# Kernel tuning notes

Measured on AMD Instinct MI355X. Metric: run time of the kernel, lower is better.

## Reference

```python
import jax, jax.numpy as jnp
import numpy as np

B, S, D, H = 2, 2048, 1024, 16
HD = D // H
NEG = -9e15


def setup_inputs() -> dict:
    key = jax.random.key(0)
    ks = jax.random.split(key, 4)
    x = jax.random.normal(ks[0], (B, S, D), dtype=jnp.float32)
    # causal mask, broadcastable over batch and heads
    mask = jnp.tril(jnp.ones((S, S), dtype=jnp.int32))[None, None]
    W_qkv = jax.random.normal(ks[1], (D, 3 * D), dtype=jnp.float32) * (1.0 / np.sqrt(D))
    b_qkv = jnp.zeros((3 * D,), dtype=jnp.float32)
    W_out = jax.random.normal(ks[2], (D, D), dtype=jnp.float32) * (1.0 / np.sqrt(D))
    b_out = jnp.zeros((D,), dtype=jnp.float32)
    return {"x": x, "mask": mask, "W_qkv": W_qkv, "b_qkv": b_qkv,
            "W_out": W_out, "b_out": b_out}


def reference(x, mask, W_qkv, b_qkv, W_out, b_out):
    b, s, _ = x.shape
    qkv = x @ W_qkv + b_qkv                       # [B,S,3D]
    qkv = qkv.reshape(b, s, H, 3 * HD)            # per-head interleaved qkv
    qkv = jnp.transpose(qkv, (0, 2, 1, 3))        # [B,H,S,3*HD]
    q, k, v = jnp.split(qkv, 3, axis=-1)          # each [B,H,S,HD]
    scores = jnp.einsum('bhqd,bhkd->bhqk', q, k) / np.sqrt(HD)
    scores = jnp.where(mask == 0, jnp.float32(NEG), scores)
    attn = jax.nn.softmax(scores, axis=-1)
    out = jnp.einsum('bhqk,bhkd->bhqd', attn, v)  # [B,H,S,HD]
    out = jnp.transpose(out, (0, 2, 1, 3)).reshape(b, s, H * HD)
    return out @ W_out + b_out
```

## Files before the change

kernel.cpp:

```cpp
#include <hip/hip_runtime.h>
#include <math.h>

constexpr int Bb = 2, Ss = 2048, Dd = 1024, Hh = 16, HDd = 64;

typedef __attribute__((ext_vector_type(8))) short bf16x8;
typedef __attribute__((ext_vector_type(4))) float f32x4;
typedef __attribute__((ext_vector_type(8))) unsigned short u16x8;
typedef __attribute__((ext_vector_type(4))) unsigned short u16x4;

__device__ __forceinline__ unsigned short bf16_rn(float f) {
  unsigned int u = __float_as_uint(f);
  u += 0x7fffu + ((u >> 16) & 1u);
  return (unsigned short)(u >> 16);
}
__device__ __forceinline__ float bf16_f(unsigned short h) {
  return __uint_as_float(((unsigned int)h) << 16);
}

__global__ __launch_bounds__(256) void split_f32(
    const float* __restrict__ in, unsigned short* __restrict__ hi,
    unsigned short* __restrict__ lo, int n8) {
  int i = blockIdx.x * 256 + threadIdx.x;
  if (i >= n8) return;
  const float4* p = (const float4*)in + (size_t)i * 2;
  float4 a = p[0], b = p[1];
  float v[8] = {a.x, a.y, a.z, a.w, b.x, b.y, b.z, b.w};
  u16x8 h, l;
  #pragma unroll
  for (int j = 0; j < 8; j++) {
    unsigned short hb = bf16_rn(v[j]);
    h[j] = hb;
    l[j] = bf16_rn(v[j] - bf16_f(hb));
  }
  *(u16x8*)(hi + (size_t)i * 8) = h;
  *(u16x8*)(lo + (size_t)i * 8) = l;
}

__global__ __launch_bounds__(256) void transpose_split_f32(
    const float* __restrict__ W, unsigned short* __restrict__ Thi,
    unsigned short* __restrict__ Tlo, int K, int N) {
  __shared__ float tile[32][33];
  int n0 = blockIdx.x * 32, k0 = blockIdx.y * 32;
  int t = threadIdx.x;
  #pragma unroll
  for (int p = 0; p < 4; p++) {
    int idx = t + p * 256;
    int kk = idx >> 5, nn = idx & 31;
    tile[kk][nn] = W[(size_t)(k0 + kk) * N + n0 + nn];
  }
  __syncthreads();
  #pragma unroll
  for (int p = 0; p < 4; p++) {
    int idx = t + p * 256;
    int nn = idx >> 5, kk = idx & 31;
    float v = tile[kk][nn];
    unsigned short hb = bf16_rn(v);
    size_t o = (size_t)(n0 + nn) * K + k0 + kk;
    Thi[o] = hb;
    Tlo[o] = bf16_rn(v - bf16_f(hb));
  }
}

typedef __attribute__((address_space(3))) unsigned int lds_u32;
typedef const __attribute__((address_space(1))) unsigned int glb_u32;
__device__ __forceinline__ void gload16(const void* g, void* l) {
  __builtin_amdgcn_global_load_lds((glb_u32*)g, (lds_u32*)l, 16, 0, 0);
}

__device__ __forceinline__ void syncb() {
  asm volatile("" ::: "memory");
  __builtin_amdgcn_s_barrier();
  asm volatile("" ::: "memory");
}
template<int N> __device__ __forceinline__ void wait_vmcnt() {
  if constexpr (N == 0)      asm volatile("s_waitcnt vmcnt(0)" ::: "memory");
  else if constexpr (N == 4) asm volatile("s_waitcnt vmcnt(4)" ::: "memory");
  else if constexpr (N == 7) asm volatile("s_waitcnt vmcnt(7)" ::: "memory");
}

template<int BM, int BN>
__device__ __forceinline__ void gemm_core256(
    const unsigned short* __restrict__ Ahi, const unsigned short* __restrict__ Alo,
    const unsigned short* __restrict__ Bhi, const unsigned short* __restrict__ Blo,
    int KD, f32x4 (&acc)[BM / 32][BN / 64])
{
  constexpr int MF = BM / 32, NF = BN / 64;
  constexpr int NA = BM / 64, NB = BN / 64;
  constexpr int NV = NA + NB;
  constexpr int AELT = 2 * BM * 32;
  constexpr int BELT = 2 * BN * 32;
  constexpr int ALO = BM * 32, BLO = BN * 32;
  __shared__ unsigned short lds[2][AELT + BELT];

  const int tid = threadIdx.x, lane = tid & 63, wid = tid >> 6;
  const int m0 = blockIdx.y * BM, n0 = blockIdx.x * BN;
  const int wrow = wid >> 2, wcol = wid & 3;
  const int lrow = lane & 15, g = lane >> 4;

  const unsigned short* srcA[NA]; int dstA[NA];
  #pragma unroll
  for (int i = 0; i < NA; i++) {
    int gi = tid + i * 512;
    int lr = gi >> 2, s = gi & 3, gs = s ^ ((lr >> 1) & 3);
    const unsigned short* bp = (lr < BM) ? Ahi : Alo;
    int row = (lr < BM) ? lr : lr - BM;
    srcA[i] = bp + (size_t)(m0 + row) * KD + gs * 8;
    dstA[i] = (gi & ~63) * 8;
  }
  const unsigned short* srcB[NB]; int dstB[NB];
  #pragma unroll
  for (int i = 0; i < NB; i++) {
    int gi = tid + i * 512;
    int lr = gi >> 2, s = gi & 3, gs = s ^ ((lr >> 1) & 3);
    const unsigned short* bp = (lr < BN) ? Bhi : Blo;
    int row = (lr < BN) ? lr : lr - BN;
    srcB[i] = bp + (size_t)(n0 + row) * KD + gs * 8;
    dstB[i] = AELT + (gi & ~63) * 8;
  }

  int offA[MF], offB[NF];
  #pragma unroll
  for (int m = 0; m < MF; m++) {
    int row = wrow * (BM / 2) + m * 16 + lrow;
    offA[m] = row * 32 + ((g ^ ((row >> 1) & 3)) * 8);
  }
  #pragma unroll
  for (int n = 0; n < NF; n++) {
    int row = wcol * (BN / 4) + n * 16 + lrow;
    offB[n] = AELT + row * 32 + ((g ^ ((row >> 1) & 3)) * 8);
  }

  #pragma unroll
  for (int m = 0; m < MF; m++)
    #pragma unroll
    for (int n = 0; n < NF; n++) acc[m][n] = (f32x4){0.f, 0.f, 0.f, 0.f};

  const int nk = KD / 32;

  #pragma unroll
  for (int i = 0; i < NA; i++) gload16(srcA[i], &lds[0][dstA[i]]);
  #pragma unroll
  for (int i = 0; i < NB; i++) gload16(srcB[i], &lds[0][dstB[i]]);
  #pragma unroll
  for (int i = 0; i < NA; i++) gload16(srcA[i] + 32, &lds[1][dstA[i]]);
  #pragma unroll
  for (int i = 0; i < NB; i++) gload16(srcB[i] + 32, &lds[1][dstB[i]]);
  wait_vmcnt<NV>();
  syncb();

  for (int t = 0; t < nk; ++t) {
    const unsigned short* L = lds[t & 1];

    bf16x8 bh[NF], bl[NF];
    #pragma unroll
    for (int n = 0; n < NF; n++) {
      bh[n] = *(const bf16x8*)(L + offB[n]);
      bl[n] = *(const bf16x8*)(L + offB[n] + BLO);
    }
    {
      bf16x8 ah[MF / 2], al[MF / 2];
      #pragma unroll
      for (int m = 0; m < MF / 2; m++) {
        ah[m] = *(const bf16x8*)(L + offA[m]);
        al[m] = *(const bf16x8*)(L + offA[m] + ALO);
      }
      __builtin_amdgcn_s_setprio(1);
      #pragma unroll
      for (int m = 0; m < MF / 2; m++)
        #pragma unroll
        for (int n = 0; n < NF; n++) {
          acc[m][n] = __builtin_amdgcn_mfma_f32_16x16x32_bf16(ah[m], bh[n], acc[m][n], 0, 0, 0);
          acc[m][n] = __builtin_amdgcn_mfma_f32_16x16x32_bf16(ah[m], bl[n], acc[m][n], 0, 0, 0);
          acc[m][n] = __builtin_amdgcn_mfma_f32_16x16x32_bf16(al[m], bh[n], acc[m][n], 0, 0, 0);
        }
      __builtin_amdgcn_s_setprio(0);
    }
    syncb();
    {
      bf16x8 ah[MF / 2], al[MF / 2];
      #pragma unroll
      for (int m = 0; m < MF / 2; m++) {
        ah[m] = *(const bf16x8*)(L + offA[m + MF / 2]);
        al[m] = *(const bf16x8*)(L + offA[m + MF / 2] + ALO);
      }
      __builtin_amdgcn_s_setprio(1);
      #pragma unroll
      for (int m = 0; m < MF / 2; m++)
        #pragma unroll
        for (int n = 0; n < NF; n++) {
          acc[m + MF / 2][n] = __builtin_amdgcn_mfma_f32_16x16x32_bf16(ah[m], bh[n], acc[m + MF / 2][n], 0, 0, 0);
          acc[m + MF / 2][n] = __builtin_amdgcn_mfma_f32_16x16x32_bf16(ah[m], bl[n], acc[m + MF / 2][n], 0, 0, 0);
          acc[m + MF / 2][n] = __builtin_amdgcn_mfma_f32_16x16x32_bf16(al[m], bh[n], acc[m + MF / 2][n], 0, 0, 0);
        }
      __builtin_amdgcn_s_setprio(0);
    }

    if (t + 1 < nk) {
      asm volatile("s_waitcnt lgkmcnt(0)" ::: "memory");
      syncb();
      if (t + 2 < nk) {
        const int koff = (t + 2) * 32;
        unsigned short* W = lds[t & 1];
        #pragma unroll
        for (int i = 0; i < NA; i++) gload16(srcA[i] + koff, W + dstA[i]);
        #pragma unroll
        for (int i = 0; i < NB; i++) gload16(srcB[i] + koff, W + dstB[i]);
        wait_vmcnt<NV>();
      } else {
        wait_vmcnt<0>();
      }
      syncb();
    }
  }
}

__global__ __launch_bounds__(512) void gemm_qkv256(
    const unsigned short* __restrict__ Ahi, const unsigned short* __restrict__ Alo,
    const unsigned short* __restrict__ Bhi, const unsigned short* __restrict__ Blo,
    const float* __restrict__ bias,
    unsigned short* __restrict__ Qh, unsigned short* __restrict__ Ql,
    unsigned short* __restrict__ Kh, unsigned short* __restrict__ Kl,
    unsigned short* __restrict__ Vth, unsigned short* __restrict__ Vtl)
{
  f32x4 acc[8][3];
  gemm_core256<256, 192>(Ahi, Alo, Bhi, Blo, 1024, acc);

  const int tid = threadIdx.x, lane = tid & 63, wid = tid >> 6;
  const int lrow = lane & 15, g = lane >> 4;
  const int m0 = blockIdx.y * 256, n0 = blockIdx.x * 192;
  const int wrow = wid >> 2, wcol = wid & 3;
  const int bidx = m0 >> 11;
  const int sbase = (m0 & 2047) + wrow * 128 + g * 4;
  #pragma unroll
  for (int n = 0; n < 3; n++) {
    int gcol = n0 + wcol * 48 + n * 16 + lrow;
    unsigned hh = (unsigned)gcol / 192u;
    int inner = gcol - (int)hh * 192;
    int part = inner >> 6;
    int d = inner & 63;
    float bv = bias[gcol];
    size_t base = (size_t)(bidx * 16 + (int)hh) * 131072;
    #pragma unroll
    for (int m = 0; m < 8; m++) {
      f32x4 a = acc[m][n];
      int s0 = sbase + m * 16;
      if (part == 0) {
        #pragma unroll
        for (int r = 0; r < 4; r++) {
          float v = (a[r] + bv) * 0.18033688011112042f;
          unsigned short hi = bf16_rn(v);
          size_t ix = base + (size_t)(s0 + r) * 64 + d;
          Qh[ix] = hi; Ql[ix] = bf16_rn(v - bf16_f(hi));
        }
      } else if (part == 1) {
        #pragma unroll
        for (int r = 0; r < 4; r++) {
          float v = a[r] + bv;
          unsigned short hi = bf16_rn(v);
          size_t ix = base + (size_t)(s0 + r) * 64 + d;
          Kh[ix] = hi; Kl[ix] = bf16_rn(v - bf16_f(hi));
        }
      } else {
        u16x4 hv, lv;
        #pragma unroll
        for (int r = 0; r < 4; r++) {
          float v = a[r] + bv;
          hv[r] = bf16_rn(v);
          lv[r] = bf16_rn(v - bf16_f(hv[r]));
        }
        size_t ix = base + (size_t)d * 2048 + s0;
        *(u16x4*)(Vth + ix) = hv;
        *(u16x4*)(Vtl + ix) = lv;
      }
    }
  }
}

__global__ __launch_bounds__(512) void gemm_out256(
    const unsigned short* __restrict__ Ahi, const unsigned short* __restrict__ Alo,
    const unsigned short* __restrict__ Bhi, const unsigned short* __restrict__ Blo,
    const float* __restrict__ bias, float* __restrict__ C)
{
  f32x4 acc[4][2];
  gemm_core256<128, 128>(Ahi, Alo, Bhi, Blo, 1024, acc);

  const int tid = threadIdx.x, lane = tid & 63, wid = tid >> 6;
  const int lrow = lane & 15, g = lane >> 4;
  const int m0 = blockIdx.y * 128, n0 = blockIdx.x * 128;
  const int wrow = wid >> 2, wcol = wid & 3;
  #pragma unroll
  for (int n = 0; n < 2; n++) {
    int gcol = n0 + wcol * 32 + n * 16 + lrow;
    float bv = bias[gcol];
    #pragma unroll
    for (int m = 0; m < 4; m++) {
      f32x4 a = acc[m][n];
      #pragma unroll
      for (int r = 0; r < 4; r++) {
        int grow = m0 + wrow * 64 + m * 16 + g * 4 + r;
        C[(size_t)grow * 1024 + gcol] = a[r] + bv;
      }
    }
  }
}

__global__ __launch_bounds__(512) void flash_attn_mfma(
    const unsigned short* __restrict__ Qh, const unsigned short* __restrict__ Ql,
    const unsigned short* __restrict__ Kh, const unsigned short* __restrict__ Kl,
    const unsigned short* __restrict__ Vth, const unsigned short* __restrict__ Vtl,
    unsigned short* __restrict__ atthi, unsigned short* __restrict__ attlo)
{
  const int pidx = blockIdx.x;
  const int h = blockIdx.y, b = blockIdx.z;
  const int bh = b * Hh + h;
  const int NT = Ss / 128;
  const int qtA = pidx, qtB = NT - 1 - pidx;
  const int tid = threadIdx.x, lane = tid & 63, wid = tid >> 6;
  const int q0w = (wid < 4) ? (qtA * 128 + wid * 32)
                            : (qtB * 128 + (wid - 4) * 32);
  const int lrow = lane & 15, lg = lane >> 4;

  __shared__ unsigned short KH[2][4096], KL[2][4096], VH[2][4096], VL[2][4096];
  __shared__ unsigned short Pbuf[8][2048];

  const size_t hb = (size_t)bh * 131072;
  const unsigned short* qhb = Qh + hb;
  const unsigned short* qlb = Ql + hb;
  const unsigned short* khb = Kh + hb;
  const unsigned short* klb = Kl + hb;
  const unsigned short* vhb = Vth + hb;
  const unsigned short* vlb = Vtl + hb;

  bf16x8 qfh[2][2], qfl[2][2];
  #pragma unroll
  for (int mi = 0; mi < 2; mi++)
    #pragma unroll
    for (int ks = 0; ks < 2; ks++) {
      int off = (q0w + mi * 16 + lrow) * 64 + ks * 32 + lg * 8;
      qfh[mi][ks] = *(const bf16x8*)(qhb + off);
      qfl[mi][ks] = *(const bf16x8*)(qlb + off);
    }

  int offK[4][2], offP[2][2];
  #pragma unroll
  for (int ci = 0; ci < 4; ci++)
    #pragma unroll
    for (int ks = 0; ks < 2; ks++) {
      int row = ci * 16 + lrow;
      offK[ci][ks] = row * 64 + (((ks * 4 + lg) ^ (row & 7)) * 8);
    }
  #pragma unroll
  for (int mi = 0; mi < 2; mi++)
    #pragma unroll
    for (int ks = 0; ks < 2; ks++) {
      int row = mi * 16 + lrow;
      offP[mi][ks] = row * 64 + (((ks * 4 + lg) ^ (row & 7)) * 8);
    }

  const int sr = tid >> 3, sg = ((tid & 7) ^ ((tid >> 3) & 7)) * 8;

  float m_[2][4], l_[2][4];
  f32x4 oacc[2][4];
  #pragma unroll
  for (int mi = 0; mi < 2; mi++)
    #pragma unroll
    for (int r = 0; r < 4; r++) { m_[mi][r] = -INFINITY; l_[mi][r] = 0.f; }
  #pragma unroll
  for (int mi = 0; mi < 2; mi++)
    #pragma unroll
    for (int di = 0; di < 4; di++) oacc[mi][di] = (f32x4){0.f, 0.f, 0.f, 0.f};

  unsigned short* Pw = Pbuf[wid];
  const int nt = 2 * (qtB + 1);

  gload16(khb + (size_t)sr * 64 + sg, KH[0] + wid * 512);
  gload16(klb + (size_t)sr * 64 + sg, KL[0] + wid * 512);
  gload16(vhb + (size_t)sr * 2048 + sg, VH[0] + wid * 512);
  gload16(vlb + (size_t)sr * 2048 + sg, VL[0] + wid * 512);
  __syncthreads();

  for (int t = 0; t < nt; ++t) {
    const int kv0 = t * 64;
    if (t + 1 < nt) {
      const int nb = (t + 1) & 1;
      const int nk = kv0 + 64;
      gload16(khb + (size_t)(nk + sr) * 64 + sg, KH[nb] + wid * 512);
      gload16(klb + (size_t)(nk + sr) * 64 + sg, KL[nb] + wid * 512);
      gload16(vhb + (size_t)sr * 2048 + nk + sg, VH[nb] + wid * 512);
      gload16(vlb + (size_t)sr * 2048 + nk + sg, VL[nb] + wid * 512);
    }

    if (kv0 <= q0w + 31) {
      const int cb = t & 1;
      const unsigned short* KHc = KH[cb];
      const unsigned short* KLc = KL[cb];
      const unsigned short* VHc = VH[cb];
      const unsigned short* VLc = VL[cb];

      f32x4 sf[2][4];
      #pragma unroll
      for (int mi = 0; mi < 2; mi++)
        #pragma unroll
        for (int ci = 0; ci < 4; ci++) sf[mi][ci] = (f32x4){0.f, 0.f, 0.f, 0.f};
      __builtin_amdgcn_s_setprio(1);
      #pragma unroll
      for (int ci = 0; ci < 4; ci++) {
        bf16x8 kh0 = *(const bf16x8*)(KHc + offK[ci][0]);
        bf16x8 kh1 = *(const bf16x8*)(KHc + offK[ci][1]);
        bf16x8 kl0 = *(const bf16x8*)(KLc + offK[ci][0]);
        bf16x8 kl1 = *(const bf16x8*)(KLc + offK[ci][1]);
        #pragma unroll
        for (int mi = 0; mi < 2; mi++) {
          f32x4 s = sf[mi][ci];
          s = __builtin_amdgcn_mfma_f32_16x16x32_bf16(qfh[mi][0], kh0, s, 0, 0, 0);
          s = __builtin_amdgcn_mfma_f32_16x16x32_bf16(qfh[mi][1], kh1, s, 0, 0, 0);
          s = __builtin_amdgcn_mfma_f32_16x16x32_bf16(qfh[mi][0], kl0, s, 0, 0, 0);
          s = __builtin_amdgcn_mfma_f32_16x16x32_bf16(qfh[mi][1], kl1, s, 0, 0, 0);
          s = __builtin_amdgcn_mfma_f32_16x16x32_bf16(qfl[mi][0], kh0, s, 0, 0, 0);
          s = __builtin_amdgcn_mfma_f32_16x16x32_bf16(qfl[mi][1], kh1, s, 0, 0, 0);
          sf[mi][ci] = s;
        }
      }
      __builtin_amdgcn_s_setprio(0);

      if (kv0 + 63 > q0w) {
        #pragma unroll
        for (int mi = 0; mi < 2; mi++)
          #pragma unroll
          for (int ci = 0; ci < 4; ci++)
            #pragma unroll
            for (int r = 0; r < 4; r++) {
              int q = q0w + mi * 16 + lg * 4 + r;
              int kv = kv0 + ci * 16 + lrow;
              if (kv > q) sf[mi][ci][r] = -1e30f;
            }
      }

      #pragma unroll
      for (int mi = 0; mi < 2; mi++)
        #pragma unroll
        for (int r = 0; r < 4; r++) {
          float mx = fmaxf(fmaxf(sf[mi][0][r], sf[mi][1][r]),
                           fmaxf(sf[mi][2][r], sf[mi][3][r]));
          mx = fmaxf(mx, __shfl_xor(mx, 1));
          mx = fmaxf(mx, __shfl_xor(mx, 2));
          mx = fmaxf(mx, __shfl_xor(mx, 4));
          mx = fmaxf(mx, __shfl_xor(mx, 8));
          float mn = fmaxf(m_[mi][r], mx);
          float alpha = __builtin_amdgcn_exp2f(m_[mi][r] - mn);
          m_[mi][r] = mn;
          float rs = 0.f;
          #pragma unroll
          for (int ci = 0; ci < 4; ci++) {
            float p = __builtin_amdgcn_exp2f(sf[mi][ci][r] - mn);
            sf[mi][ci][r] = p;
            rs += p;
          }
          rs += __shfl_xor(rs, 1);
          rs += __shfl_xor(rs, 2);
          rs += __shfl_xor(rs, 4);
          rs += __shfl_xor(rs, 8);
          l_[mi][r] = l_[mi][r] * alpha + rs;
          #pragma unroll
          for (int di = 0; di < 4; di++) oacc[mi][di][r] *= alpha;
        }

      #pragma unroll
      for (int mi = 0; mi < 2; mi++)
        #pragma unroll
        for (int ci = 0; ci < 4; ci++) {
          int colb = ci * 16 + lrow;
          int gcol = colb >> 3, crem = colb & 7;
          #pragma unroll
          for (int r = 0; r < 4; r++) {
            int rr = mi * 16 + lg * 4 + r;
            Pw[rr * 64 + ((gcol ^ (rr & 7)) * 8) + crem] = bf16_rn(sf[mi][ci][r]);
          }
        }

      bf16x8 pa[2][2];
      #pragma unroll
      for (int mi = 0; mi < 2; mi++)
        #pragma unroll
        for (int ks = 0; ks < 2; ks++)
          pa[mi][ks] = *(const bf16x8*)(Pw + offP[mi][ks]);
      __builtin_amdgcn_s_setprio(1);
      #pragma unroll
      for (int di = 0; di < 4; di++) {
        bf16x8 vh0 = *(const bf16x8*)(VHc + offK[di][0]);
        bf16x8 vh1 = *(const bf16x8*)(VHc + offK[di][1]);
        bf16x8 vl0 = *(const bf16x8*)(VLc + offK[di][0]);
        bf16x8 vl1 = *(const bf16x8*)(VLc + offK[di][1]);
        #pragma unroll
        for (int mi = 0; mi < 2; mi++) {
          f32x4 o = oacc[mi][di];
          o = __builtin_amdgcn_mfma_f32_16x16x32_bf16(pa[mi][0], vh0, o, 0, 0, 0);
          o = __builtin_amdgcn_mfma_f32_16x16x32_bf16(pa[mi][1], vh1, o, 0, 0, 0);
          o = __builtin_amdgcn_mfma_f32_16x16x32_bf16(pa[mi][0], vl0, o, 0, 0, 0);
          o = __builtin_amdgcn_mfma_f32_16x16x32_bf16(pa[mi][1], vl1, o, 0, 0, 0);
          oacc[mi][di] = o;
        }
      }
      __builtin_amdgcn_s_setprio(0);
    }
    __syncthreads();
  }

  #pragma unroll
  for (int mi = 0; mi < 2; mi++) {
    float inv[4];
    #pragma unroll
    for (int r = 0; r < 4; r++) inv[r] = 1.f / l_[mi][r];
    #pragma unroll
    for (int di = 0; di < 4; di++) {
      f32x4 o = oacc[mi][di];
      #pragma unroll
      for (int r = 0; r < 4; r++) {
        float v = o[r] * inv[r];
        int srow = q0w + mi * 16 + lg * 4 + r;
        size_t idx = ((size_t)b * Ss + srow) * 1024 + h * 64 + di * 16 + lrow;
        unsigned short hi = bf16_rn(v);
        atthi[idx] = hi;
        attlo[idx] = bf16_rn(v - bf16_f(hi));
      }
    }
  }
}

extern "C" void kernel_launch(void* const* d_in, const int* in_sizes, int n_in,
                              void* d_out, int out_size, void* d_ws, size_t ws_size,
                              hipStream_t stream) {
  const float* x    = (const float*)d_in[0];
  const float* Wqkv = (const float*)d_in[2];
  const float* bqkv = (const float*)d_in[3];
  const float* Wout = (const float*)d_in[4];
  const float* bout = (const float*)d_in[5];
  float* out = (float*)d_out;

  char* ws = (char*)d_ws;
  unsigned short* Qh  = (unsigned short*)(ws);
  unsigned short* Ql  = (unsigned short*)(ws + 8388608);
  unsigned short* Kh  = (unsigned short*)(ws + 16777216);
  unsigned short* Kl  = (unsigned short*)(ws + 25165824);
  unsigned short* Vth = (unsigned short*)(ws + 33554432);
  unsigned short* Vtl = (unsigned short*)(ws + 41943040);
  unsigned short* atthi = (unsigned short*)(ws + 50331648);
  unsigned short* attlo = (unsigned short*)(ws + 58720256);
  unsigned short* xhi = (unsigned short*)(ws + 67108864);
  unsigned short* xlo = (unsigned short*)(ws + 75497472);
  unsigned short* wqh = (unsigned short*)(ws + 83886080);
  unsigned short* wql = (unsigned short*)(ws + 90177536);
  unsigned short* woh = (unsigned short*)(ws + 96468992);
  unsigned short* wol = (unsigned short*)(ws + 98566144);

  const int M = Bb * Ss;

  split_f32<<<(M * Dd / 8) / 256, 256, 0, stream>>>(x, xhi, xlo, M * Dd / 8);
  transpose_split_f32<<<dim3(3 * Dd / 32, Dd / 32), 256, 0, stream>>>(Wqkv, wqh, wql, Dd, 3 * Dd);
  transpose_split_f32<<<dim3(Dd / 32, Dd / 32), 256, 0, stream>>>(Wout, woh, wol, Dd, Dd);

  gemm_qkv256<<<dim3(16, 16), 512, 0, stream>>>(
      xhi, xlo, wqh, wql, bqkv, Qh, Ql, Kh, Kl, Vth, Vtl);

  flash_attn_mfma<<<dim3(Ss / 256, Hh, Bb), 512, 0, stream>>>(
      Qh, Ql, Kh, Kl, Vth, Vtl, atthi, attlo);

  gemm_out256<<<dim3(8, 32), 512, 0, stream>>>(
      atthi, attlo, woh, wol, bout, out);
}
```

Before: 312.3 us.

## Read V straight from global memory and compute softmax row sums with MFMA

V hi/lo tiles are no longer staged through double-buffered shared memory. Each wave loads its V fragments directly from global memory (expected to hit in cache), which halves LDS use and allows a launch bound of 4 blocks per CU. The row-sum of P is now taken with an MFMA against a ones vector instead of VALU adds and shuffle reductions, so it sums the bf16-rounded P values. In exchange, per-wave global loads now sit on the critical path of the PV MFMAs and could add latency.

Result: slower. 667.1 us (+113.6%).

```diff
diff --git a/kernel.cpp b/kernel.cpp
--- a/kernel.cpp
+++ b/kernel.cpp
@@ -304,7 +304,7 @@
   }
 }
 
-__global__ __launch_bounds__(512) void flash_attn_mfma(
+__global__ __launch_bounds__(512, 4) void flash_attn_mfma(
     const unsigned short* __restrict__ Qh, const unsigned short* __restrict__ Ql,
     const unsigned short* __restrict__ Kh, const unsigned short* __restrict__ Kl,
     const unsigned short* __restrict__ Vth, const unsigned short* __restrict__ Vtl,
@@ -320,7 +320,7 @@
                             : (qtB * 128 + (wid - 4) * 32);
   const int lrow = lane & 15, lg = lane >> 4;
 
-  __shared__ unsigned short KH[2][4096], KL[2][4096], VH[2][4096], VL[2][4096];
+  __shared__ unsigned short KH[2][4096], KL[2][4096];
   __shared__ unsigned short Pbuf[8][2048];
 
   const size_t hb = (size_t)bh * 131072;
@@ -341,6 +341,10 @@
       qfl[mi][ks] = *(const bf16x8*)(qlb + off);
     }
 
+  bf16x8 onesf;
+  #pragma unroll
+  for (int j = 0; j < 8; j++) onesf[j] = (short)0x3F80;
+
   int offK[4][2], offP[2][2];
   #pragma unroll
   for (int ci = 0; ci < 4; ci++)
@@ -357,26 +361,28 @@
       offP[mi][ks] = row * 64 + (((ks * 4 + lg) ^ (row & 7)) * 8);
     }
 
+  const unsigned short* vhrow = vhb + (size_t)lrow * 2048 + lg * 8;
+  const unsigned short* vlrow = vlb + (size_t)lrow * 2048 + lg * 8;
+
   const int sr = tid >> 3, sg = ((tid & 7) ^ ((tid >> 3) & 7)) * 8;
 
-  float m_[2][4], l_[2][4];
+  float m_[2][4];
+  f32x4 lacc[2];
   f32x4 oacc[2][4];
   #pragma unroll
-  for (int mi = 0; mi < 2; mi++)
-    #pragma unroll
-    for (int r = 0; r < 4; r++) { m_[mi][r] = -INFINITY; l_[mi][r] = 0.f; }
-  #pragma unroll
-  for (int mi = 0; mi < 2; mi++)
+  for (int mi = 0; mi < 2; mi++) {
+    lacc[mi] = (f32x4){0.f, 0.f, 0.f, 0.f};
+    #pragma unroll
+    for (int r = 0; r < 4; r++) m_[mi][r] = -INFINITY;
     #pragma unroll
     for (int di = 0; di < 4; di++) oacc[mi][di] = (f32x4){0.f, 0.f, 0.f, 0.f};
+  }
 
   unsigned short* Pw = Pbuf[wid];
   const int nt = 2 * (qtB + 1);
 
   gload16(khb + (size_t)sr * 64 + sg, KH[0] + wid * 512);
   gload16(klb + (size_t)sr * 64 + sg, KL[0] + wid * 512);
-  gload16(vhb + (size_t)sr * 2048 + sg, VH[0] + wid * 512);
-  gload16(vlb + (size_t)sr * 2048 + sg, VL[0] + wid * 512);
   __syncthreads();
 
   for (int t = 0; t < nt; ++t) {
@@ -386,16 +392,12 @@
       const int nk = kv0 + 64;
       gload16(khb + (size_t)(nk + sr) * 64 + sg, KH[nb] + wid * 512);
       gload16(klb + (size_t)(nk + sr) * 64 + sg, KL[nb] + wid * 512);
-      gload16(vhb + (size_t)sr * 2048 + nk + sg, VH[nb] + wid * 512);
-      gload16(vlb + (size_t)sr * 2048 + nk + sg, VL[nb] + wid * 512);
     }
 
     if (kv0 <= q0w + 31) {
       const int cb = t & 1;
       const unsigned short* KHc = KH[cb];
       const unsigned short* KLc = KL[cb];
-      const unsigned short* VHc = VH[cb];
-      const unsigned short* VLc = VL[cb];
 
       f32x4 sf[2][4];
       #pragma unroll
@@ -449,18 +451,10 @@
           float mn = fmaxf(m_[mi][r], mx);
           float alpha = __builtin_amdgcn_exp2f(m_[mi][r] - mn);
           m_[mi][r] = mn;
-          float rs = 0.f;
           #pragma unroll
-          for (int ci = 0; ci < 4; ci++) {
-            float p = __builtin_amdgcn_exp2f(sf[mi][ci][r] - mn);
-            sf[mi][ci][r] = p;
-            rs += p;
-          }
-          rs += __shfl_xor(rs, 1);
-          rs += __shfl_xor(rs, 2);
-          rs += __shfl_xor(rs, 4);
-          rs += __shfl_xor(rs, 8);
-          l_[mi][r] = l_[mi][r] * alpha + rs;
+          for (int ci = 0; ci < 4; ci++)
+            sf[mi][ci][r] = __builtin_amdgcn_exp2f(sf[mi][ci][r] - mn);
+          lacc[mi][r] *= alpha;
           #pragma unroll
           for (int di = 0; di < 4; di++) oacc[mi][di][r] *= alpha;
         }
@@ -484,13 +478,22 @@
         #pragma unroll
         for (int ks = 0; ks < 2; ks++)
           pa[mi][ks] = *(const bf16x8*)(Pw + offP[mi][ks]);
+
+      #pragma unroll
+      for (int mi = 0; mi < 2; mi++) {
+        lacc[mi] = __builtin_amdgcn_mfma_f32_16x16x32_bf16(pa[mi][0], onesf, lacc[mi], 0, 0, 0);
+        lacc[mi] = __builtin_amdgcn_mfma_f32_16x16x32_bf16(pa[mi][1], onesf, lacc[mi], 0, 0, 0);
+      }
+
       __builtin_amdgcn_s_setprio(1);
       #pragma unroll
       for (int di = 0; di < 4; di++) {
-        bf16x8 vh0 = *(const bf16x8*)(VHc + offK[di][0]);
-        bf16x8 vh1 = *(const bf16x8*)(VHc + offK[di][1]);
-        bf16x8 vl0 = *(const bf16x8*)(VLc + offK[di][0]);
-        bf16x8 vl1 = *(const bf16x8*)(VLc + offK[di][1]);
+        const unsigned short* vh = vhrow + (size_t)(di * 16) * 2048 + kv0;
+        const unsigned short* vl = vlrow + (size_t)(di * 16) * 2048 + kv0;
+        bf16x8 vh0 = *(const bf16x8*)(vh);
+        bf16x8 vh1 = *(const bf16x8*)(vh + 32);
+        bf16x8 vl0 = *(const bf16x8*)(vl);
+        bf16x8 vl1 = *(const bf16x8*)(vl + 32);
         #pragma unroll
         for (int mi = 0; mi < 2; mi++) {
           f32x4 o = oacc[mi][di];
@@ -510,7 +513,7 @@
   for (int mi = 0; mi < 2; mi++) {
     float inv[4];
     #pragma unroll
-    for (int r = 0; r < 4; r++) inv[r] = 1.f / l_[mi][r];
+    for (int r = 0; r < 4; r++) inv[r] = 1.f / lacc[mi][r];
     #pragma unroll
     for (int di = 0; di < 4; di++) {
       f32x4 o = oacc[mi][di];
```

## Single-buffer V in flash attention, loading it during QK^T with split waits

Applied to the files above, without the earlier changes.

V tiles are no longer double-buffered. Each iteration now issues the current V tile's global-to-LDS load at its start, alongside the prefetch of the next K tile. Explicit vmcnt waits and barriers are placed so that QK^T and the softmax overlap the V load, and a third barrier protects the single V buffer before it is overwritten. This frees LDS, which may allow more blocks per CU. The cost is an extra barrier per iteration and less prefetch distance for V, which may expose load latency.

Result: no change. 312.7 us (+0.1%).

```diff
diff --git a/kernel.cpp b/kernel.cpp
--- a/kernel.cpp
+++ b/kernel.cpp
@@ -74,6 +74,7 @@
 }
 template<int N> __device__ __forceinline__ void wait_vmcnt() {
   if constexpr (N == 0)      asm volatile("s_waitcnt vmcnt(0)" ::: "memory");
+  else if constexpr (N == 2) asm volatile("s_waitcnt vmcnt(2)" ::: "memory");
   else if constexpr (N == 4) asm volatile("s_waitcnt vmcnt(4)" ::: "memory");
   else if constexpr (N == 7) asm volatile("s_waitcnt vmcnt(7)" ::: "memory");
 }
@@ -320,7 +321,8 @@
                             : (qtB * 128 + (wid - 4) * 32);
   const int lrow = lane & 15, lg = lane >> 4;
 
-  __shared__ unsigned short KH[2][4096], KL[2][4096], VH[2][4096], VL[2][4096];
+  __shared__ unsigned short KH[2][4096], KL[2][4096];
+  __shared__ unsigned short VH[4096], VL[4096];
   __shared__ unsigned short Pbuf[8][2048];
 
   const size_t hb = (size_t)bh * 131072;
@@ -375,29 +377,32 @@
 
   gload16(khb + (size_t)sr * 64 + sg, KH[0] + wid * 512);
   gload16(klb + (size_t)sr * 64 + sg, KL[0] + wid * 512);
-  gload16(vhb + (size_t)sr * 2048 + sg, VH[0] + wid * 512);
-  gload16(vlb + (size_t)sr * 2048 + sg, VL[0] + wid * 512);
-  __syncthreads();
 
   for (int t = 0; t < nt; ++t) {
     const int kv0 = t * 64;
-    if (t + 1 < nt) {
+    const bool haveK = (t + 1 < nt);
+
+    gload16(vhb + (size_t)sr * 2048 + kv0 + sg, VH + wid * 512);
+    gload16(vlb + (size_t)sr * 2048 + kv0 + sg, VL + wid * 512);
+    if (haveK) {
       const int nb = (t + 1) & 1;
       const int nk = kv0 + 64;
       gload16(khb + (size_t)(nk + sr) * 64 + sg, KH[nb] + wid * 512);
       gload16(klb + (size_t)(nk + sr) * 64 + sg, KL[nb] + wid * 512);
-      gload16(vhb + (size_t)sr * 2048 + nk + sg, VH[nb] + wid * 512);
-      gload16(vlb + (size_t)sr * 2048 + nk + sg, VL[nb] + wid * 512);
-    }
-
-    if (kv0 <= q0w + 31) {
-      const int cb = t & 1;
+      wait_vmcnt<4>();
+    } else {
+      wait_vmcnt<2>();
+    }
+    syncb();
+
+    const int cb = t & 1;
+    const bool active = (kv0 <= q0w + 31);
+
+    f32x4 sf[2][4];
+    if (active) {
       const unsigned short* KHc = KH[cb];
       const unsigned short* KLc = KL[cb];
-      const unsigned short* VHc = VH[cb];
-      const unsigned short* VLc = VL[cb];
-
-      f32x4 sf[2][4];
+
       #pragma unroll
       for (int mi = 0; mi < 2; mi++)
         #pragma unroll
@@ -477,7 +482,12 @@
             Pw[rr * 64 + ((gcol ^ (rr & 7)) * 8) + crem] = bf16_rn(sf[mi][ci][r]);
           }
         }
-
+    }
+
+    if (haveK) wait_vmcnt<2>(); else wait_vmcnt<0>();
+    syncb();
+
+    if (active) {
       bf16x8 pa[2][2];
       #pragma unroll
       for (int mi = 0; mi < 2; mi++)
@@ -487,10 +497,10 @@
       __builtin_amdgcn_s_setprio(1);
       #pragma unroll
       for (int di = 0; di < 4; di++) {
-        bf16x8 vh0 = *(const bf16x8*)(VHc + offK[di][0]);
-        bf16x8 vh1 = *(const bf16x8*)(VHc + offK[di][1]);
-        bf16x8 vl0 = *(const bf16x8*)(VLc + offK[di][0]);
-        bf16x8 vl1 = *(const bf16x8*)(VLc + offK[di][1]);
+        bf16x8 vh0 = *(const bf16x8*)(VH + offK[di][0]);
+        bf16x8 vh1 = *(const bf16x8*)(VH + offK[di][1]);
+        bf16x8 vl0 = *(const bf16x8*)(VL + offK[di][0]);
+        bf16x8 vl1 = *(const bf16x8*)(VL + offK[di][1]);
         #pragma unroll
         for (int mi = 0; mi < 2; mi++) {
           f32x4 o = oacc[mi][di];
@@ -502,8 +512,9 @@
         }
       }
       __builtin_amdgcn_s_setprio(0);
-    }
-    __syncthreads();
+      asm volatile("s_waitcnt lgkmcnt(0)" ::: "memory");
+    }
+    syncb();
   }
 
   #pragma unroll
```
